# Performance work log

Measured on AMD Instinct MI355X. Metric: run time of the kernel, lower is better.

The kernel has to match this reference:

```python
import jax, jax.numpy as jnp
import numpy as np

B, S, D = 1, 2048, 1024
HK, DK = 8, 64
HV, DV = 16, 64
KEY_DIM = HK * DK          # 512
VAL_DIM = HV * DV          # 1024
CONV_DIM = 2 * KEY_DIM + VAL_DIM  # 2048
KW = 4                     # conv kernel width
E, TOPK, I_MOE = 8, 2, 512
EPS = 1e-6


def rms_norm(x, w, eps=EPS):
    xf = x.astype(jnp.float32)
    y = xf * jax.lax.rsqrt(jnp.mean(xf * xf, axis=-1, keepdims=True) + eps)
    return (y * (1.0 + w.astype(jnp.float32))).astype(x.dtype)


def l2norm(x, eps=1e-6):
    return x * jax.lax.rsqrt(jnp.sum(x * x, axis=-1, keepdims=True) + eps)


def setup_inputs() -> dict:
    key = jax.random.key(0)
    ks = jax.random.split(key, 16)
    n = lambda k, shp, s=0.02: (jax.random.normal(k, shp, dtype=jnp.float32) * s)
    return {
        'x': jax.random.normal(ks[0], (B, S, D), dtype=jnp.float32),
        'state': jnp.zeros((B, HV, DK, DV), dtype=jnp.float32),
        'conv_state': jnp.zeros((B, KW - 1, CONV_DIM), dtype=jnp.float32),
        'in_proj_qkv': n(ks[1], (D, CONV_DIM)),
        'in_proj_z': n(ks[2], (D, VAL_DIM)),
        'in_proj_a': n(ks[3], (D, HV)),
        'in_proj_b': n(ks[4], (D, HV)),
        'conv1d_weight': n(ks[5], (CONV_DIM, KW)),
        'dt_bias': jnp.ones((HV,), dtype=jnp.float32),
        'A_log': jnp.zeros((HV,), dtype=jnp.float32),
        'norm_weight': jnp.zeros((VAL_DIM,), dtype=jnp.float32),
        'out_proj': n(ks[6], (VAL_DIM, D)),
        'router_weight': n(ks[7], (E, D)),
        'expert_gate_up': n(ks[8], (E, 2 * I_MOE, D)),
        'expert_down': n(ks[9], (E, D, I_MOE)),
        'shared_gate': n(ks[10], (D, VAL_DIM)),
        'shared_up': n(ks[11], (D, VAL_DIM)),
        'shared_down': n(ks[12], (VAL_DIM, D)),
        'shared_expert_gate': n(ks[13], (D, 1)),
        'attention_norm_weight': jnp.zeros((D,), dtype=jnp.float32),
        'ffn_norm_weight': jnp.zeros((D,), dtype=jnp.float32),
        'linear_layer_idx': 0,
    }


def reference(x, state, conv_state, in_proj_qkv, in_proj_z, in_proj_a, in_proj_b,
              conv1d_weight, dt_bias, A_log, norm_weight, out_proj,
              router_weight, expert_gate_up, expert_down, shared_gate, shared_up,
              shared_down, shared_expert_gate, attention_norm_weight,
              ffn_norm_weight, linear_layer_idx):
    bsz, seqlen, dim = x.shape
    h = rms_norm(x, attention_norm_weight)

    # ---- Gated DeltaNet linear attention (prefill) ----
    qkv = h @ in_proj_qkv                    # [B,S,CONV_DIM]
    z = h @ in_proj_z                        # [B,S,VAL_DIM]
    a = h @ in_proj_a                        # [B,S,HV]
    b = h @ in_proj_b                        # [B,S,HV]

    # causal depthwise conv1d with rolling cache, then SiLU
    seq = jnp.concatenate([conv_state, qkv], axis=1)     # [B,S+KW-1,C]
    new_conv_state = seq[:, -(KW - 1):, :]
    xc = jnp.swapaxes(seq, 1, 2)                         # [B,C,S+KW-1]
    wk = conv1d_weight[:, None, :]                       # [C,1,KW]
    conv = jax.lax.conv_general_dilated(
        xc, wk, window_strides=(1,), padding='VALID',
        dimension_numbers=('NCH', 'OIH', 'NCH'), feature_group_count=CONV_DIM)
    qkv = jax.nn.silu(jnp.swapaxes(conv, 1, 2))          # [B,S,C]

    q, k, v = jnp.split(qkv, [KEY_DIM, 2 * KEY_DIM], axis=-1)
    q = l2norm(q.reshape(bsz, seqlen, HK, DK))
    k = l2norm(k.reshape(bsz, seqlen, HK, DK))
    rep = HV // HK
    q = jnp.repeat(q, rep, axis=2) * (DK ** -0.5)        # [B,S,HV,DK]
    k = jnp.repeat(k, rep, axis=2)
    v = v.reshape(bsz, seqlen, HV, DV)

    beta = jax.nn.sigmoid(b)                             # [B,S,HV]
    g = -jnp.exp(A_log) * jax.nn.softplus(a + dt_bias)   # log decay
    decay = jnp.exp(g)                                   # [B,S,HV]

    def step(St, inp):
        qt, kt, vt, dt_, bt = inp                        # per-token slices
        St = St * dt_[..., None, None]                   # gated decay
        mem = jnp.einsum('bhk,bhkv->bhv', kt, St)        # retrieve
        delta = (vt - mem) * bt[..., None]               # delta rule
        St = St + jnp.einsum('bhk,bhv->bhkv', kt, delta)
        ot = jnp.einsum('bhk,bhkv->bhv', qt, St)
        return St, ot

    xs = (jnp.moveaxis(q, 1, 0), jnp.moveaxis(k, 1, 0), jnp.moveaxis(v, 1, 0),
          jnp.moveaxis(decay, 1, 0), jnp.moveaxis(beta, 1, 0))
    new_state, o = jax.lax.scan(step, state, xs)
    o = jnp.moveaxis(o, 0, 1)                            # [B,S,HV,DV]

    # gated RMSNorm per value head, gate = silu(z)
    nw = (1.0 + norm_weight.astype(jnp.float32)).reshape(HV, DV)
    of = o.astype(jnp.float32)
    of = of * jax.lax.rsqrt(jnp.mean(of * of, axis=-1, keepdims=True) + EPS) * nw
    o = (of * jax.nn.silu(z.reshape(bsz, seqlen, HV, DV).astype(jnp.float32))).astype(x.dtype)
    attn_out = o.reshape(bsz, seqlen, VAL_DIM) @ out_proj
    x = x + attn_out

    # ---- MoE FFN with shared expert ----
    hf = rms_norm(x, ffn_norm_weight)
    t = hf.reshape(-1, dim)                              # [T,D]
    T = t.shape[0]
    logits = t @ router_weight.T                         # [T,E]
    probs = jax.nn.softmax(logits.astype(jnp.float32), axis=-1)
    vals, idx = jax.lax.top_k(probs, TOPK)
    vals = vals / jnp.sum(vals, axis=-1, keepdims=True)  # renormalized top-k
    wdense = jnp.zeros((T, E), jnp.float32).at[jnp.arange(T)[:, None], idx].set(vals)

    gu = jnp.einsum('td,eid->tei', t, expert_gate_up)    # [T,E,2I]
    gate, up = jnp.split(gu, 2, axis=-1)
    act = jax.nn.silu(gate) * up                         # [T,E,I]
    eo = jnp.einsum('tei,edi->ted', act, expert_down)    # [T,E,D]
    routed = jnp.einsum('ted,te->td', eo, wdense.astype(eo.dtype))

    sh = (jax.nn.silu(t @ shared_gate) * (t @ shared_up)) @ shared_down
    sh = sh * jax.nn.sigmoid(t @ shared_expert_gate)

    moe_out = (routed + sh).reshape(bsz, seqlen, dim)
    x = x + moe_out
    return x, new_state, new_conv_state
```

## Files before the change

### kernel.cpp

```cpp
#include <hip/hip_runtime.h>
#include <stdint.h>

typedef _Float16 f16;
typedef __attribute__((ext_vector_type(8))) _Float16 f16x8;
typedef __attribute__((ext_vector_type(4))) float f32x4;

#define DEV static __device__ __forceinline__

DEV float siluf(float x){ return x/(1.f+expf(-x)); }

__global__ __launch_bounds__(256)
void prep_kernel(const float* __restrict__ qkvw, const float* __restrict__ zw,
                 const float* __restrict__ opw, const float* __restrict__ sgw,
                 const float* __restrict__ suw, const float* __restrict__ sdw,
                 const float* __restrict__ guw, const float* __restrict__ dww,
                 f16* __restrict__ wqkvz, f16* __restrict__ wop, f16* __restrict__ wsgu,
                 f16* __restrict__ wsd, f16* __restrict__ wgu, f16* __restrict__ wdn)
{
  int b = blockIdx.x, tid = threadIdx.x;
  if (b >= 7168){
    if (b < 9216){
      size_t base = ((size_t)(b-7168))*4096 + (size_t)tid*16;
      long e = base>>20; long i = (base>>10)&1023; long d = base&1023;
      long ri = (i<512) ? ((i>>6)*128 + (i&63)) : (((i&511)>>6)*128 + 64 + (i&63));
      size_t dbase = ((size_t)e<<20) + ((size_t)ri<<10) + d;
      #pragma unroll
      for (int u=0;u<16;u++) wgu[dbase+u] = (f16)guw[base+u];
    } else {
      size_t base = ((size_t)(b-9216))*4096 + (size_t)tid*16;
      #pragma unroll
      for (int u=0;u<16;u++) wdn[base+u] = (f16)dww[base+u];
    }
    return;
  }
  const float* src; f16* dst; int N; int rowOff; int tile; int mode=0;
  if (b < 2048){ src=qkvw; dst=wqkvz; N=2048; rowOff=0;    tile=b; }
  else if (b < 3072){ src=zw;  dst=wqkvz; N=1024; rowOff=2048; tile=b-2048; }
  else if (b < 4096){ src=opw; dst=wop;  N=1024; rowOff=0;    tile=b-3072; }
  else if (b < 5120){ src=sgw; dst=wsgu; N=1024; rowOff=0;    tile=b-4096; mode=1; }
  else if (b < 6144){ src=suw; dst=wsgu; N=1024; rowOff=0;    tile=b-5120; mode=2; }
  else              { src=sdw; dst=wsd;  N=1024; rowOff=0;    tile=b-6144; }
  __shared__ float t32[32][33];
  int ntiles = N/32;
  int k0 = (tile/ntiles)*32, n0 = (tile%ntiles)*32;
  int rr = tid>>5, cc = tid&31;
  #pragma unroll
  for (int u=0;u<4;u++) t32[rr+u*8][cc] = src[(size_t)(k0+rr+u*8)*N + n0+cc];
  __syncthreads();
  #pragma unroll
  for (int u=0;u<4;u++){
    int vr = n0 + rr + u*8;
    int drow = rowOff + vr;
    if (mode==1) drow = (vr>>6)*128 + (vr&63);
    else if (mode==2) drow = (vr>>6)*128 + 64 + (vr&63);
    dst[(size_t)drow*1024 + k0+cc] = (f16)t32[cc][rr+u*8];
  }
}

__global__ __launch_bounds__(256)
void rms1(const float* __restrict__ xin, const float* __restrict__ w, f16* __restrict__ hb)
{
  __shared__ float red[4];
  int t = blockIdx.x, tid = threadIdx.x;
  const float* row = xin + (long)t*1024;
  float vals[4]; float ss=0.f;
  #pragma unroll
  for (int u=0;u<4;u++){ vals[u]=row[tid+256*u]; ss += vals[u]*vals[u]; }
  #pragma unroll
  for (int m=1;m<64;m<<=1) ss += __shfl_xor(ss,m);
  if ((tid&63)==0) red[tid>>6]=ss;
  __syncthreads();
  float sc = rsqrtf((red[0]+red[1]+red[2]+red[3])*(1.f/1024.f) + 1e-6f);
  #pragma unroll
  for (int u=0;u<4;u++){
    int d = tid+256*u;
    hb[(long)t*1024+d] = (f16)(vals[u]*sc*(1.f+w[d]));
  }
}

__global__ __launch_bounds__(256)
void rms2(const float* __restrict__ xin, const float* __restrict__ w,
          f16* __restrict__ hb, float* __restrict__ hf, int* __restrict__ cnt)
{
  __shared__ float red[4];
  int t = blockIdx.x, tid = threadIdx.x;
  if (blockIdx.x==0 && tid<8) cnt[tid]=0;
  const float* row = xin + (long)t*1024;
  float vals[4]; float ss=0.f;
  #pragma unroll
  for (int u=0;u<4;u++){ vals[u]=row[tid+256*u]; ss += vals[u]*vals[u]; }
  #pragma unroll
  for (int m=1;m<64;m<<=1) ss += __shfl_xor(ss,m);
  if ((tid&63)==0) red[tid>>6]=ss;
  __syncthreads();
  float sc = rsqrtf((red[0]+red[1]+red[2]+red[3])*(1.f/1024.f) + 1e-6f);
  #pragma unroll
  for (int u=0;u<4;u++){
    int d = tid+256*u;
    float v = vals[u]*sc*(1.f+w[d]);
    hb[(long)t*1024+d] = (f16)v;
    hf[(long)t*1024+d] = v;
  }
}

constexpr int GM_PLAIN=0, GM_ADDX=1, GM_GUF=2, GM_DOWN=3, GM_SHD=4, GM_SGUF=5;

template<int MODE>
__global__ __launch_bounds__(256)
void gemm_k(const f16* __restrict__ A, long strideA,
            const f16* __restrict__ B, long strideB,
            int K, int lda, int ldb,
            float* __restrict__ Cf, f16* __restrict__ Cb, int ldc, long strideCb,
            const float* __restrict__ xadd,
            const int* __restrict__ tok, const int* __restrict__ cntp,
            const int* __restrict__ slot, const float* __restrict__ wgt,
            const float* __restrict__ sig)
{
  constexpr bool FUSED = (MODE==GM_GUF || MODE==GM_SGUF);
  __shared__ f16 As[128*64];
  __shared__ f16 Bs[128*64];
  __shared__ int ltok[128];
  const int e = blockIdx.z;
  const int m0 = blockIdx.y*128, n0 = blockIdx.x*128;
  int cnt = 0x7fffffff;
  if (MODE==GM_GUF || MODE==GM_DOWN){
    cnt = cntp[e];
    if (m0 >= cnt) return;
  }
  const f16* Ap = A + (long)e*strideA;
  const f16* Bp = B + (long)e*strideB;
  const int tid = threadIdx.x, lane = tid&63, wv = tid>>6;
  if (MODE==GM_GUF){
    if (tid < 128){
      int p = m0 + tid;
      ltok[tid] = (p < cnt) ? tok[e*2048 + p] : 0;
    }
  }
  __syncthreads();
  const int srow = wv*8 + (lane>>3);
  const int scol = (lane&7)*8;
  long arow[4];
  #pragma unroll
  for (int i=0;i<4;i++){
    int r = srow + i*32;
    arow[i] = (MODE==GM_GUF) ? (long)ltok[r] : (long)(m0 + r);
  }
  f32x4 acc[4][4];
  #pragma unroll
  for (int mi=0;mi<4;mi++)
    #pragma unroll
    for (int ni=0;ni<4;ni++)
      acc[mi][ni] = (f32x4){0.f,0.f,0.f,0.f};

  for (int k0=0;k0<K;k0+=64){
    f16x8 av[4], bv[4];
    #pragma unroll
    for (int i=0;i<4;i++){
      int r = srow + i*32;
      av[i] = *(const f16x8*)(Ap + arow[i]*lda + k0 + scol);
      bv[i] = *(const f16x8*)(Bp + (long)(n0 + r)*ldb + k0 + scol);
    }
    __syncthreads();
    #pragma unroll
    for (int i=0;i<4;i++){
      int r = srow + i*32;
      *(f16x8*)&As[r*64 + scol] = av[i];
      *(f16x8*)&Bs[r*64 + scol] = bv[i];
    }
    __syncthreads();
    #pragma unroll
    for (int kk=0;kk<64;kk+=32){
      f16x8 af[4], bf[4];
      #pragma unroll
      for (int mi=0;mi<4;mi++){
        int row = (wv&1)*64 + mi*16 + (lane&15);
        af[mi] = *(const f16x8*)&As[row*64 + kk + (lane>>4)*8];
      }
      #pragma unroll
      for (int ni=0;ni<4;ni++){
        int row = FUSED ? (ni*32 + (wv>>1)*16 + (lane&15))
                        : ((wv>>1)*64 + ni*16 + (lane&15));
        bf[ni] = *(const f16x8*)&Bs[row*64 + kk + (lane>>4)*8];
      }
      #pragma unroll
      for (int mi=0;mi<4;mi++)
        #pragma unroll
        for (int ni=0;ni<4;ni++)
          acc[mi][ni] = __builtin_amdgcn_mfma_f32_16x16x32_f16(af[mi], bf[ni], acc[mi][ni], 0,0,0);
    }
  }
  if (FUSED){
    #pragma unroll
    for (int mi=0;mi<4;mi++){
      #pragma unroll
      for (int r=0;r<4;r++){
        int rowl = (wv&1)*64 + mi*16 + (lane>>4)*4 + r;
        int pos = m0 + rowl;
        #pragma unroll
        for (int pi=0;pi<2;pi++){
          int v = (n0>>1) + pi*32 + (wv>>1)*16 + (lane&15);
          float g = acc[mi][pi][r], u = acc[mi][pi+2][r];
          f16 a = (f16)(siluf(g)*u);
          if (MODE==GM_GUF) Cb[(long)e*strideCb + (long)pos*ldc + v] = a;
          else              Cb[(long)pos*ldc + v] = a;
        }
      }
    }
  } else {
    #pragma unroll
    for (int mi=0;mi<4;mi++){
      #pragma unroll
      for (int r=0;r<4;r++){
        int rowl = (wv&1)*64 + mi*16 + (lane>>4)*4 + r;
        int pos = m0 + rowl;
        int tk=0, sl=0; float wrow=0.f;
        if (MODE==GM_DOWN){
          if (pos < cnt){ tk = tok[e*2048+pos]; sl = slot[e*2048+pos]; wrow = wgt[e*2048+pos]; }
        }
        #pragma unroll
        for (int ni=0;ni<4;ni++){
          int col = n0 + (wv>>1)*64 + ni*16 + (lane&15);
          float v = acc[mi][ni][r];
          if (MODE==GM_PLAIN){
            Cf[(long)pos*ldc + col] = v;
          } else if (MODE==GM_ADDX){
            long idx = (long)pos*ldc + col;
            Cf[idx] = v + xadd[idx];
          } else if (MODE==GM_DOWN){
            if (pos < cnt) Cf[(long)sl*2097152 + (long)tk*1024 + col] = v*wrow;
          } else {
            Cf[(long)pos*ldc + col] = v*sig[pos];
          }
        }
      }
    }
  }
}

__global__ __launch_bounds__(256)
void ab_kernel(const f16* __restrict__ hb, const float* __restrict__ Wa,
               const float* __restrict__ Wbp, const float* __restrict__ dtb,
               const float* __restrict__ alog,
               float* __restrict__ gg, float* __restrict__ bbet)
{
  __shared__ float hrow[1024];
  __shared__ float part[256];
  int t = blockIdx.x, tid = threadIdx.x;
  #pragma unroll
  for (int u=0;u<4;u++){ int d = tid+256*u; hrow[d] = (float)hb[(long)t*1024+d]; }
  __syncthreads();
  int o = tid & 31;
  int r = tid >> 5;
  const float* W = (o<16) ? Wa : Wbp;
  int col = o & 15;
  float s = 0.f;
  for (int d=r; d<1024; d+=8) s += hrow[d]*W[d*16+col];
  part[tid] = s;
  __syncthreads();
  if (tid < 32){
    float tot=0.f;
    #pragma unroll
    for (int q=0;q<8;q++) tot += part[q*32 + tid];
    if (tid<16){
      float a = tot + dtb[tid];
      float sp = (a>20.f)? a : log1pf(expf(a));
      gg[t*16+tid] = -expf(alog[tid])*sp;
    } else {
      bbet[t*16+(tid-16)] = 1.f/(1.f+expf(-tot));
    }
  }
}

__global__ __launch_bounds__(256)
void conv_kernel(const float* __restrict__ qkvz, const float* __restrict__ cs,
                 const float* __restrict__ cw,
                 float* __restrict__ qn, float* __restrict__ kn,
                 float* __restrict__ vb, float* __restrict__ conv_out)
{
  int t = blockIdx.y;
  int c = blockIdx.x*256 + threadIdx.x;
  f32x4 w4 = *(const f32x4*)&cw[c*4];
  float acc = 0.f;
  #pragma unroll
  for (int j=0;j<4;j++){
    int s = t + j;
    float xv = (s<3) ? cs[s*2048 + c] : qkvz[(long)(s-3)*3072 + c];
    acc += w4[j]*xv;
  }
  float sv = siluf(acc);
  if (c < 1024){
    float ssq = sv*sv;
    #pragma unroll
    for (int m=1;m<64;m<<=1) ssq += __shfl_xor(ssq, m);
    float y = sv*rsqrtf(ssq + 1e-6f);
    if (c < 512) qn[(long)t*512 + c] = y*0.125f;
    else         kn[(long)t*512 + (c-512)] = y;
  } else {
    vb[(long)t*1024 + (c-1024)] = sv;
  }
  if (t >= 2045) conv_out[(t-2045)*2048 + c] = qkvz[(long)t*3072 + c];
}

__global__ __launch_bounds__(256)
void scan_pre(const float* __restrict__ kn, const float* __restrict__ vg,
              const float* __restrict__ gg, const float* __restrict__ bb,
              float* __restrict__ U0, f16* __restrict__ WbB,
              float* __restrict__ MT, float* __restrict__ NT)
{
  __shared__ f16 Kh[64][72];
  __shared__ f16 KrT[64][72];
  __shared__ f16 Amh[64][72];
  __shared__ float XT[64][68];
  __shared__ f16 Xh[64][72];
  __shared__ float cexp[64], gam[64], rlast[64], betl[64];
  const int task = blockIdx.x;
  const int h = task>>5, c = task&31, hk = h>>1;
  const int tid = threadIdx.x, lane = tid&63, wv = tid>>6;
  const long tb = (long)task*4096;

  if (wv==0){
    float g = gg[(c*64+lane)*16 + h];
    #pragma unroll
    for (int off=1; off<64; off<<=1){
      float tpp = __shfl_up(g, off);
      if (lane >= off) g += tpp;
    }
    cexp[lane] = g;
    betl[lane] = bb[(c*64+lane)*16 + h];
  }
  __syncthreads();
  if (tid<64){ gam[tid]=expf(cexp[tid]); rlast[tid]=expf(cexp[63]-cexp[tid]); }
  __syncthreads();
  for (int u=0;u<16;u++){
    int e2=u*256+tid; int t=e2>>6, x=e2&63;
    float kx = kn[(long)(c*64+t)*512 + hk*64 + x];
    Kh[t][x] = (f16)kx;
    KrT[x][t] = (f16)(rlast[t]*kx);
  }
  __syncthreads();
  {
    int mt = wv;
    for (int nt=0;nt<4;nt++){
      f32x4 acc = {0.f,0.f,0.f,0.f};
      #pragma unroll
      for (int kk=0;kk<64;kk+=32){
        f16x8 a = *(const f16x8*)&Kh[mt*16 + (lane&15)][kk + (lane>>4)*8];
        f16x8 bB = *(const f16x8*)&Kh[nt*16 + (lane&15)][kk + (lane>>4)*8];
        acc = __builtin_amdgcn_mfma_f32_16x16x32_f16(a, bB, acc, 0,0,0);
      }
      #pragma unroll
      for (int r=0;r<4;r++){
        int t = mt*16 + (lane>>4)*4 + r;
        int i = nt*16 + (lane&15);
        float v = (i<t) ? betl[t]*expf(cexp[t]-cexp[i])*acc[r] : 0.f;
        Amh[t][i] = (f16)v;
      }
    }
  }

  for (int pass=0; pass<2; pass++){
    for (int u=0;u<18;u++) ((f16*)Xh)[u*256+tid] = (f16)0.f;
    for (int u=0;u<16;u++){
      int e2=u*256+tid; int t=e2>>6, col=e2&63;
      float v = (pass==0) ? betl[t]*vg[(long)(c*64+t)*1024 + h*64 + col]
                          : betl[t]*gam[t]*kn[(long)(c*64+t)*512 + hk*64 + col];
      XT[col][t] = v;
    }
    __syncthreads();

    for (int b4=0;b4<4;b4++){
      if (tid<64){
        int col = tid;
        float xr[16];
        #pragma unroll
        for (int j=0;j<16;j+=4){
          f32x4 v = *(const f32x4*)&XT[col][b4*16+j];
          xr[j]=v.x; xr[j+1]=v.y; xr[j+2]=v.z; xr[j+3]=v.w;
        }
        #pragma unroll
        for (int t=1;t<16;t++){
          float a = xr[t];
          #pragma unroll
          for (int i=0;i<t;i++) a -= (float)Amh[b4*16+t][b4*16+i]*xr[i];
          xr[t] = a;
        }
        #pragma unroll
        for (int j=0;j<16;j+=4)
          *(f32x4*)&XT[col][b4*16+j] = (f32x4){xr[j],xr[j+1],xr[j+2],xr[j+3]};
        f16x8 h0, h1;
        #pragma unroll
        for (int j=0;j<8;j++){ h0[j]=(f16)xr[j]; h1[j]=(f16)xr[8+j]; }
        *(f16x8*)&Xh[col][b4*16]   = h0;
        *(f16x8*)&Xh[col][b4*16+8] = h1;
        if (pass==0){
          #pragma unroll
          for (int j=0;j<16;j++) U0[tb + (b4*16+j)*64 + col] = xr[j];
        } else {
          #pragma unroll
          for (int j=0;j<16;j++) WbB[tb + (b4*16+j)*64 + col] = (f16)xr[j];
        }
      }
      __syncthreads();
      if (b4<3){
        int ntiles = 4*(3-b4);
        for (int idx=wv; idx<ntiles; idx+=4){
          int mtile = idx & 3;
          int ntile = idx >> 2;
          int tp0 = 16*(b4+1) + ntile*16;
          f16x8 a  = *(const f16x8*)&Xh[mtile*16 + (lane&15)][b4*16 + (lane>>4)*8];
          f16x8 bB = *(const f16x8*)&Amh[tp0 + (lane&15)][b4*16 + (lane>>4)*8];
          f32x4 acc = {0.f,0.f,0.f,0.f};
          acc = __builtin_amdgcn_mfma_f32_16x16x32_f16(a, bB, acc, 0,0,0);
          #pragma unroll
          for (int r=0;r<4;r++){
            int colr = mtile*16 + (lane>>4)*4 + r;
            int tp = tp0 + (lane&15);
            XT[colr][tp] -= acc[r];
          }
        }
      }
      __syncthreads();
    }
    for (int idx=wv; idx<16; idx+=4){
      int mtile = idx & 3, ntile = idx >> 2;
      f32x4 acc = {0.f,0.f,0.f,0.f};
      #pragma unroll
      for (int kk=0;kk<64;kk+=32){
        f16x8 a  = *(const f16x8*)&Xh[mtile*16 + (lane&15)][kk + (lane>>4)*8];
        f16x8 bB = *(const f16x8*)&KrT[ntile*16 + (lane&15)][kk + (lane>>4)*8];
        acc = __builtin_amdgcn_mfma_f32_16x16x32_f16(a, bB, acc, 0,0,0);
      }
      #pragma unroll
      for (int r=0;r<4;r++){
        int m = mtile*16 + (lane>>4)*4 + r;
        int n = ntile*16 + (lane&15);
        if (pass==0) NT[tb + m*64 + n] = acc[r];
        else         MT[tb + m*64 + n] = ((n==m)?gam[63]:0.f) - acc[r];
      }
    }
    __syncthreads();
  }
}

__global__ __launch_bounds__(256)
void scan_seq(const float* __restrict__ st_in, const float* __restrict__ MT,
              const float* __restrict__ NT, float* __restrict__ SS,
              float* __restrict__ st_out)
{
  __shared__ float Mb[2][64*64];
  __shared__ float Nb[2][16*64];
  __shared__ float Sl[64][16];
  const int h = blockIdx.x>>2, vgq = blockIdx.x&3;
  const int tid = threadIdx.x, lane = tid&63, wv = tid>>6;
  const long hb0 = (long)h*32*4096;
  {
    int kx = tid>>2, j0 = (tid&3)*4;
    f32x4 s = *(const f32x4*)&st_in[h*4096 + kx*64 + vgq*16 + j0];
    *(f32x4*)&Sl[kx][j0] = s;
  }
  f32x4 mreg[4]; f32x4 nreg;
  #pragma unroll
  for (int u=0;u<4;u++) mreg[u] = *(const f32x4*)&MT[hb0 + (u*256+tid)*4];
  nreg = *(const f32x4*)&NT[hb0 + vgq*1024 + tid*4];
  #pragma unroll
  for (int u=0;u<4;u++) *(f32x4*)&Mb[0][(u*256+tid)*4] = mreg[u];
  *(f32x4*)&Nb[0][tid*4] = nreg;
  __syncthreads();

  const int kx = tid>>2, j0 = (tid&3)*4;
  for (int c=0;c<32;c++){
    const int buf = c&1;
    const long tb = hb0 + (long)c*4096;
    *(f32x4*)&SS[tb + kx*64 + vgq*16 + j0] = *(const f32x4*)&Sl[kx][j0];
    if (c<31){
      const long tb1 = tb + 4096;
      #pragma unroll
      for (int u=0;u<4;u++) mreg[u] = *(const f32x4*)&MT[tb1 + (u*256+tid)*4];
      nreg = *(const f32x4*)&NT[tb1 + vgq*1024 + tid*4];
    }
    f32x4 acc = {0.f,0.f,0.f,0.f};
    #pragma unroll 16
    for (int b=0;b<64;b++){
      float m = Mb[buf][b*64 + lane];
      f32x4 s4 = *(const f32x4*)&Sl[b][wv*4];
      acc.x += m*s4.x; acc.y += m*s4.y; acc.z += m*s4.z; acc.w += m*s4.w;
    }
    __syncthreads();
    Sl[lane][wv*4+0] = acc.x + Nb[buf][(wv*4+0)*64 + lane];
    Sl[lane][wv*4+1] = acc.y + Nb[buf][(wv*4+1)*64 + lane];
    Sl[lane][wv*4+2] = acc.z + Nb[buf][(wv*4+2)*64 + lane];
    Sl[lane][wv*4+3] = acc.w + Nb[buf][(wv*4+3)*64 + lane];
    if (c<31){
      #pragma unroll
      for (int u=0;u<4;u++) *(f32x4*)&Mb[buf^1][(u*256+tid)*4] = mreg[u];
      *(f32x4*)&Nb[buf^1][tid*4] = nreg;
    }
    __syncthreads();
  }
  *(f32x4*)&st_out[h*4096 + kx*64 + vgq*16 + j0] = *(const f32x4*)&Sl[kx][j0];
}

__global__ __launch_bounds__(256)
void scan_out(const float* __restrict__ qn, const float* __restrict__ kn,
              const float* __restrict__ gg, const float* __restrict__ U0,
              const f16* __restrict__ WbB, const float* __restrict__ SS,
              const float* __restrict__ qkvz, const float* __restrict__ nw,
              f16* __restrict__ obuf)
{
  __shared__ f16 Kh[64][72];
  __shared__ f16 Qh[64][72];
  __shared__ f16 Wbh[64][72];
  __shared__ f16 Bmh[64][72];
  __shared__ f16 STh[64][72];
  __shared__ f16 UTh[64][72];
  __shared__ float cexp[64], gam[64];
  const int task = blockIdx.x;
  const int h = task>>5, c = task&31, hk = h>>1;
  const int tid = threadIdx.x, lane = tid&63, wv = tid>>6;
  const long tb = (long)task*4096;

  if (wv==0){
    float g = gg[(c*64+lane)*16 + h];
    #pragma unroll
    for (int off=1; off<64; off<<=1){
      float tpp = __shfl_up(g, off);
      if (lane >= off) g += tpp;
    }
    cexp[lane]=g; gam[lane]=expf(g);
  }
  __syncthreads();
  for (int u=0;u<16;u++){
    int e2=u*256+tid; int t=e2>>6, x=e2&63;
    float kx = kn[(long)(c*64+t)*512 + hk*64 + x];
    float qx = qn[(long)(c*64+t)*512 + hk*64 + x];
    Kh[t][x]=(f16)kx;
    Qh[t][x]=(f16)qx;
    Wbh[t][x] = WbB[tb + t*64 + x];
    STh[x][t] = (f16)SS[tb + t*64 + x];
  }
  __syncthreads();
  {
    int mt = wv;
    for (int nt=0;nt<4;nt++){
      f32x4 acc={0.f,0.f,0.f,0.f};
      #pragma unroll
      for (int kk=0;kk<64;kk+=32){
        f16x8 a  = *(const f16x8*)&Qh[mt*16+(lane&15)][kk+(lane>>4)*8];
        f16x8 bB = *(const f16x8*)&Kh[nt*16+(lane&15)][kk+(lane>>4)*8];
        acc = __builtin_amdgcn_mfma_f32_16x16x32_f16(a,bB,acc,0,0,0);
      }
      #pragma unroll
      for (int r=0;r<4;r++){
        int t = mt*16+(lane>>4)*4+r;
        int i = nt*16+(lane&15);
        float v = (i<=t)? expf(cexp[t]-cexp[i])*acc[r] : 0.f;
        Bmh[t][i] = (f16)v;
      }
    }
  }
  __syncthreads();
  {
    int mt = wv;
    for (int nt=0;nt<4;nt++){
      f32x4 acc={0.f,0.f,0.f,0.f};
      #pragma unroll
      for (int kk=0;kk<64;kk+=32){
        f16x8 a  = *(const f16x8*)&Wbh[mt*16+(lane&15)][kk+(lane>>4)*8];
        f16x8 bB = *(const f16x8*)&STh[nt*16+(lane&15)][kk+(lane>>4)*8];
        acc = __builtin_amdgcn_mfma_f32_16x16x32_f16(a,bB,acc,0,0,0);
      }
      #pragma unroll
      for (int r=0;r<4;r++){
        int t = mt*16+(lane>>4)*4+r;
        int v = nt*16+(lane&15);
        float uv = U0[tb + t*64 + v] - acc[r];
        UTh[v][t] = (f16)uv;
      }
    }
    for (int u=0;u<16;u++){
      int e2=u*256+tid; int t=e2>>6, x=e2&63;
      Qh[t][x] = (f16)(gam[t]*(float)Qh[t][x]);
    }
  }
  __syncthreads();
  {
    int mt = wv;
    f32x4 acc[4];
    for (int nt=0;nt<4;nt++){
      acc[nt]=(f32x4){0.f,0.f,0.f,0.f};
      #pragma unroll
      for (int kk=0;kk<64;kk+=32){
        f16x8 a  = *(const f16x8*)&Qh[mt*16+(lane&15)][kk+(lane>>4)*8];
        f16x8 bB = *(const f16x8*)&STh[nt*16+(lane&15)][kk+(lane>>4)*8];
        acc[nt] = __builtin_amdgcn_mfma_f32_16x16x32_f16(a,bB,acc[nt],0,0,0);
      }
      #pragma unroll
      for (int kk=0;kk<64;kk+=32){
        f16x8 a  = *(const f16x8*)&Bmh[mt*16+(lane&15)][kk+(lane>>4)*8];
        f16x8 bB = *(const f16x8*)&UTh[nt*16+(lane&15)][kk+(lane>>4)*8];
        acc[nt] = __builtin_amdgcn_mfma_f32_16x16x32_f16(a,bB,acc[nt],0,0,0);
      }
    }
    #pragma unroll
    for (int r=0;r<4;r++){
      float ss = acc[0][r]*acc[0][r] + acc[1][r]*acc[1][r]
               + acc[2][r]*acc[2][r] + acc[3][r]*acc[3][r];
      ss += __shfl_xor(ss,1); ss += __shfl_xor(ss,2);
      ss += __shfl_xor(ss,4); ss += __shfl_xor(ss,8);
      float scale = rsqrtf(ss*(1.f/64.f) + 1e-6f);
      int t = mt*16 + (lane>>4)*4 + r;
      int tg = c*64 + t;
      #pragma unroll
      for (int nt=0;nt<4;nt++){
        int v = nt*16 + (lane&15);
        float z = qkvz[(long)tg*3072 + 2048 + h*64 + v];
        float val = acc[nt][r]*scale*(1.f+nw[h*64+v])*siluf(z);
        obuf[(long)tg*1024 + h*64 + v] = (f16)val;
      }
    }
  }
}

__global__ __launch_bounds__(64)
void router_k(const float* __restrict__ hff, const float* __restrict__ rw,
              const float* __restrict__ seg,
              int* __restrict__ cnt, int* __restrict__ etok, int* __restrict__ eslot,
              float* __restrict__ ew, float* __restrict__ sig)
{
  int t = blockIdx.x; int lane = threadIdx.x;
  const float* row = hff + (long)t*1024;
  float p[9];
  #pragma unroll
  for (int e=0;e<9;e++) p[e]=0.f;
  for (int rdx=0; rdx<16; rdx++){
    int d = lane + 64*rdx;
    float xv = row[d];
    #pragma unroll
    for (int e=0;e<8;e++) p[e] += xv*rw[e*1024+d];
    p[8] += xv*seg[d];
  }
  #pragma unroll
  for (int e=0;e<9;e++)
    #pragma unroll
    for (int m=1;m<64;m<<=1) p[e] += __shfl_xor(p[e], m);
  if (lane==0){
    float mx = p[0];
    for (int e=1;e<8;e++) mx = fmaxf(mx,p[e]);
    float pe[8];
    for (int e=0;e<8;e++) pe[e]=expf(p[e]-mx);
    int i0=0; for (int e=1;e<8;e++) if (pe[e]>pe[i0]) i0=e;
    int i1 = (i0==0)?1:0;
    for (int e=0;e<8;e++) if (e!=i0 && pe[e]>pe[i1]) i1=e;
    float denom = pe[i0]+pe[i1];
    float w0 = pe[i0]/denom, w1 = pe[i1]/denom;
    int p0 = atomicAdd(&cnt[i0],1);
    etok[i0*2048+p0]=t; eslot[i0*2048+p0]=0; ew[i0*2048+p0]=w0;
    int p1 = atomicAdd(&cnt[i1],1);
    etok[i1*2048+p1]=t; eslot[i1*2048+p1]=1; ew[i1*2048+p1]=w1;
    sig[t] = 1.f/(1.f+expf(-p[8]));
  }
}

__global__ __launch_bounds__(256)
void fin_kernel(const float* __restrict__ x2, const float* __restrict__ eo2,
                const float* __restrict__ sh, float* __restrict__ outx)
{
  long idx = (long)blockIdx.x*256 + threadIdx.x;
  outx[idx] = x2[idx] + eo2[idx] + eo2[idx + 2097152] + sh[idx];
}

extern "C" void kernel_launch(void* const* d_in, const int* in_sizes, int n_in,
                              void* d_out, int out_size, void* d_ws, size_t ws_size,
                              hipStream_t stream)
{
  (void)in_sizes; (void)n_in; (void)out_size; (void)ws_size;
  const float* x      = (const float*)d_in[0];
  const float* state  = (const float*)d_in[1];
  const float* cstate = (const float*)d_in[2];
  const float* w_qkv  = (const float*)d_in[3];
  const float* w_z    = (const float*)d_in[4];
  const float* w_a    = (const float*)d_in[5];
  const float* w_b    = (const float*)d_in[6];
  const float* convw  = (const float*)d_in[7];
  const float* dtb    = (const float*)d_in[8];
  const float* alog   = (const float*)d_in[9];
  const float* normw  = (const float*)d_in[10];
  const float* w_op   = (const float*)d_in[11];
  const float* rw     = (const float*)d_in[12];
  const float* w_gu   = (const float*)d_in[13];
  const float* w_dn   = (const float*)d_in[14];
  const float* w_sg   = (const float*)d_in[15];
  const float* w_su   = (const float*)d_in[16];
  const float* w_sd   = (const float*)d_in[17];
  const float* w_seg  = (const float*)d_in[18];
  const float* anw    = (const float*)d_in[19];
  const float* fnw    = (const float*)d_in[20];

  char* ws = (char*)d_ws;
  size_t off = 0;
  auto alloc = [&](size_t bytes)->char*{
    char* p = ws + off; off += (bytes + 255) & ~(size_t)255; return p;
  };
  f16*  wTqkvz = (f16*)alloc((size_t)3072*1024*2);
  f16*  wTop   = (f16*)alloc((size_t)1024*1024*2);
  f16*  wTsgu  = (f16*)alloc((size_t)2048*1024*2);
  f16*  wTsd   = (f16*)alloc((size_t)1024*1024*2);
  f16*  wGUc   = (f16*)alloc((size_t)8*1024*1024*2);
  f16*  wDNc   = (f16*)alloc((size_t)8*1024*512*2);
  f16*  hbuf   = (f16*)alloc((size_t)2048*1024*2);
  float* qkvz  = (float*)alloc((size_t)2048*3072*4);
  float* qn    = (float*)alloc((size_t)2048*512*4);
  float* kn    = (float*)alloc((size_t)2048*512*4);
  float* vb    = (float*)alloc((size_t)2048*1024*4);
  float* gg    = (float*)alloc((size_t)2048*16*4);
  float* bbuf  = (float*)alloc((size_t)2048*16*4);
  float* U0    = (float*)alloc((size_t)512*4096*4);
  f16*  WbB    = (f16*)alloc((size_t)512*4096*2);
  float* MT    = (float*)alloc((size_t)512*4096*4);
  float* NT    = (float*)alloc((size_t)512*4096*4);
  float* SS    = (float*)alloc((size_t)512*4096*4);
  float* x2    = (float*)alloc((size_t)2048*1024*4);
  f16*  hfb    = (f16*)alloc((size_t)2048*1024*2);
  float* hff   = (float*)alloc((size_t)2048*1024*4);
  int*  cnt    = (int*)alloc(256);
  int*  etok   = (int*)alloc((size_t)8*2048*4);
  int*  eslot  = (int*)alloc((size_t)8*2048*4);
  float* ew    = (float*)alloc((size_t)8*2048*4);
  float* sigb  = (float*)alloc((size_t)2048*4);
  f16*  obuf  = hbuf;
  f16*  sactb = (f16*)qn;
  float* shb  = vb;
  f16*  actb  = (f16*)U0;
  float* eo2  = (float*)((char*)U0 + (size_t)16777216);

  float* out_x = (float*)d_out;
  float* out_state = out_x + 2097152;
  float* out_conv = out_state + 65536;

  prep_kernel<<<10240, 256, 0, stream>>>(w_qkv, w_z, w_op, w_sg, w_su, w_sd, w_gu, w_dn,
                                         wTqkvz, wTop, wTsgu, wTsd, wGUc, wDNc);
  rms1<<<2048, 256, 0, stream>>>(x, anw, hbuf);
  gemm_k<GM_PLAIN><<<dim3(24,16,1), 256, 0, stream>>>(hbuf, 0, wTqkvz, 0, 1024, 1024, 1024,
        qkvz, nullptr, 3072, 0, nullptr, nullptr, nullptr, nullptr, nullptr, nullptr);
  ab_kernel<<<2048, 256, 0, stream>>>(hbuf, w_a, w_b, dtb, alog, gg, bbuf);
  conv_kernel<<<dim3(8,2048), 256, 0, stream>>>(qkvz, cstate, convw, qn, kn, vb, out_conv);
  scan_pre<<<512, 256, 0, stream>>>(kn, vb, gg, bbuf, U0, WbB, MT, NT);
  scan_seq<<<64, 256, 0, stream>>>(state, MT, NT, SS, out_state);
  scan_out<<<512, 256, 0, stream>>>(qn, kn, gg, U0, WbB, SS, qkvz, normw, obuf);
  gemm_k<GM_ADDX><<<dim3(8,16,1), 256, 0, stream>>>(obuf, 0, wTop, 0, 1024, 1024, 1024,
        x2, nullptr, 1024, 0, x, nullptr, nullptr, nullptr, nullptr, nullptr);
  rms2<<<2048, 256, 0, stream>>>(x2, fnw, hfb, hff, cnt);
  router_k<<<2048, 64, 0, stream>>>(hff, rw, w_seg, cnt, etok, eslot, ew, sigb);
  gemm_k<GM_GUF><<<dim3(8,16,8), 256, 0, stream>>>(hfb, 0, wGUc, (long)1024*1024, 1024, 1024, 1024,
        nullptr, actb, 512, (long)2048*512, nullptr, etok, cnt, nullptr, nullptr, nullptr);
  gemm_k<GM_DOWN><<<dim3(8,16,8), 256, 0, stream>>>(actb, (long)2048*512, wDNc, (long)1024*512,
        512, 512, 512,
        eo2, nullptr, 1024, 0, nullptr, etok, cnt, eslot, ew, nullptr);
  gemm_k<GM_SGUF><<<dim3(16,16,1), 256, 0, stream>>>(hfb, 0, wTsgu, 0, 1024, 1024, 1024,
        nullptr, sactb, 1024, 0, nullptr, nullptr, nullptr, nullptr, nullptr, nullptr);
  gemm_k<GM_SHD><<<dim3(8,16,1), 256, 0, stream>>>(sactb, 0, wTsd, 0, 1024, 1024, 1024,
        shb, nullptr, 1024, 0, nullptr, nullptr, nullptr, nullptr, nullptr, sigb);
  fin_kernel<<<8192, 256, 0, stream>>>(x2, eo2, shb, out_x);
}
```

Baseline: 540.5 us.

## Fuse router into second RMSNorm and stage GEMM tiles via direct global-to-LDS loads

Merges the MoE router (logits, softmax, top-2, token bucketing, shared-expert sigmoid) into the rms2 kernel. This removes one launch and the fp32 normalized-activation round trip through global memory, and the counter reset moves to a memset. The GEMM kernel now uses global_load_lds to copy A/B tiles straight into LDS instead of going through registers, which cuts register pressure and VGPR traffic. Each k-step still has two barriers and there is no double buffering, so load latency is still not overlapped.

```diff
diff --git a/kernel.cpp b/kernel.cpp
--- a/kernel.cpp
+++ b/kernel.cpp
@@ -8,6 +8,12 @@
 #define DEV static __device__ __forceinline__
 
 DEV float siluf(float x){ return x/(1.f+expf(-x)); }
+
+DEV void load_lds16(const f16* g, f16* l){
+  __builtin_amdgcn_global_load_lds(
+      (const __attribute__((address_space(1))) void*)g,
+      (__attribute__((address_space(3))) void*)l, 16, 0, 0);
+}
 
 __global__ __launch_bounds__(256)
 void prep_kernel(const float* __restrict__ qkvw, const float* __restrict__ zw,
@@ -80,26 +86,62 @@
 
 __global__ __launch_bounds__(256)
 void rms2(const float* __restrict__ xin, const float* __restrict__ w,
-          f16* __restrict__ hb, float* __restrict__ hf, int* __restrict__ cnt)
+          const float* __restrict__ rw, const float* __restrict__ seg,
+          f16* __restrict__ hb,
+          int* __restrict__ cnt, int* __restrict__ etok, int* __restrict__ eslot,
+          float* __restrict__ ew, float* __restrict__ sig)
 {
   __shared__ float red[4];
-  int t = blockIdx.x, tid = threadIdx.x;
-  if (blockIdx.x==0 && tid<8) cnt[tid]=0;
+  __shared__ float rbuf[9][4];
+  int t = blockIdx.x, tid = threadIdx.x, lane = tid&63, wv = tid>>6;
   const float* row = xin + (long)t*1024;
   float vals[4]; float ss=0.f;
   #pragma unroll
   for (int u=0;u<4;u++){ vals[u]=row[tid+256*u]; ss += vals[u]*vals[u]; }
   #pragma unroll
   for (int m=1;m<64;m<<=1) ss += __shfl_xor(ss,m);
-  if ((tid&63)==0) red[tid>>6]=ss;
+  if (lane==0) red[wv]=ss;
   __syncthreads();
   float sc = rsqrtf((red[0]+red[1]+red[2]+red[3])*(1.f/1024.f) + 1e-6f);
+  float p[9];
+  #pragma unroll
+  for (int e=0;e<9;e++) p[e]=0.f;
   #pragma unroll
   for (int u=0;u<4;u++){
     int d = tid+256*u;
     float v = vals[u]*sc*(1.f+w[d]);
     hb[(long)t*1024+d] = (f16)v;
-    hf[(long)t*1024+d] = v;
+    #pragma unroll
+    for (int e=0;e<8;e++) p[e] += v*rw[e*1024+d];
+    p[8] += v*seg[d];
+  }
+  #pragma unroll
+  for (int e=0;e<9;e++)
+    #pragma unroll
+    for (int m=1;m<64;m<<=1) p[e] += __shfl_xor(p[e], m);
+  if (lane==0){
+    #pragma unroll
+    for (int e=0;e<9;e++) rbuf[e][wv]=p[e];
+  }
+  __syncthreads();
+  if (tid==0){
+    float pl[9];
+    #pragma unroll
+    for (int e=0;e<9;e++) pl[e]=rbuf[e][0]+rbuf[e][1]+rbuf[e][2]+rbuf[e][3];
+    float mx = pl[0];
+    for (int e=1;e<8;e++) mx = fmaxf(mx,pl[e]);
+    float pe[8];
+    for (int e=0;e<8;e++) pe[e]=expf(pl[e]-mx);
+    int i0=0; for (int e=1;e<8;e++) if (pe[e]>pe[i0]) i0=e;
+    int i1 = (i0==0)?1:0;
+    for (int e=0;e<8;e++) if (e!=i0 && pe[e]>pe[i1]) i1=e;
+    float denom = pe[i0]+pe[i1];
+    float w0 = pe[i0]/denom, w1 = pe[i1]/denom;
+    int p0 = atomicAdd(&cnt[i0],1);
+    etok[i0*2048+p0]=t; eslot[i0*2048+p0]=0; ew[i0*2048+p0]=w0;
+    int p1 = atomicAdd(&cnt[i1],1);
+    etok[i1*2048+p1]=t; eslot[i1*2048+p1]=1; ew[i1*2048+p1]=w1;
+    sig[t] = 1.f/(1.f+expf(-pl[8]));
   }
 }
 
@@ -135,8 +177,8 @@
       int p = m0 + tid;
       ltok[tid] = (p < cnt) ? tok[e*2048 + p] : 0;
     }
-  }
-  __syncthreads();
+    __syncthreads();
+  }
   const int srow = wv*8 + (lane>>3);
   const int scol = (lane&7)*8;
   long arow[4];
@@ -153,19 +195,12 @@
       acc[mi][ni] = (f32x4){0.f,0.f,0.f,0.f};
 
   for (int k0=0;k0<K;k0+=64){
-    f16x8 av[4], bv[4];
+    __syncthreads();
     #pragma unroll
     for (int i=0;i<4;i++){
       int r = srow + i*32;
-      av[i] = *(const f16x8*)(Ap + arow[i]*lda + k0 + scol);
-      bv[i] = *(const f16x8*)(Bp + (long)(n0 + r)*ldb + k0 + scol);
-    }
-    __syncthreads();
-    #pragma unroll
-    for (int i=0;i<4;i++){
-      int r = srow + i*32;
-      *(f16x8*)&As[r*64 + scol] = av[i];
-      *(f16x8*)&Bs[r*64 + scol] = bv[i];
+      load_lds16(Ap + arow[i]*lda + k0 + scol, &As[r*64 + scol]);
+      load_lds16(Bp + (long)(n0 + r)*ldb + k0 + scol, &Bs[r*64 + scol]);
     }
     __syncthreads();
     #pragma unroll
@@ -621,46 +656,6 @@
   }
 }
 
-__global__ __launch_bounds__(64)
-void router_k(const float* __restrict__ hff, const float* __restrict__ rw,
-              const float* __restrict__ seg,
-              int* __restrict__ cnt, int* __restrict__ etok, int* __restrict__ eslot,
-              float* __restrict__ ew, float* __restrict__ sig)
-{
-  int t = blockIdx.x; int lane = threadIdx.x;
-  const float* row = hff + (long)t*1024;
-  float p[9];
-  #pragma unroll
-  for (int e=0;e<9;e++) p[e]=0.f;
-  for (int rdx=0; rdx<16; rdx++){
-    int d = lane + 64*rdx;
-    float xv = row[d];
-    #pragma unroll
-    for (int e=0;e<8;e++) p[e] += xv*rw[e*1024+d];
-    p[8] += xv*seg[d];
-  }
-  #pragma unroll
-  for (int e=0;e<9;e++)
-    #pragma unroll
-    for (int m=1;m<64;m<<=1) p[e] += __shfl_xor(p[e], m);
-  if (lane==0){
-    float mx = p[0];
-    for (int e=1;e<8;e++) mx = fmaxf(mx,p[e]);
-    float pe[8];
-    for (int e=0;e<8;e++) pe[e]=expf(p[e]-mx);
-    int i0=0; for (int e=1;e<8;e++) if (pe[e]>pe[i0]) i0=e;
-    int i1 = (i0==0)?1:0;
-    for (int e=0;e<8;e++) if (e!=i0 && pe[e]>pe[i1]) i1=e;
-    float denom = pe[i0]+pe[i1];
-    float w0 = pe[i0]/denom, w1 = pe[i1]/denom;
-    int p0 = atomicAdd(&cnt[i0],1);
-    etok[i0*2048+p0]=t; eslot[i0*2048+p0]=0; ew[i0*2048+p0]=w0;
-    int p1 = atomicAdd(&cnt[i1],1);
-    etok[i1*2048+p1]=t; eslot[i1*2048+p1]=1; ew[i1*2048+p1]=w1;
-    sig[t] = 1.f/(1.f+expf(-p[8]));
-  }
-}
-
 __global__ __launch_bounds__(256)
 void fin_kernel(const float* __restrict__ x2, const float* __restrict__ eo2,
                 const float* __restrict__ sh, float* __restrict__ outx)
@@ -721,7 +716,6 @@
   float* SS    = (float*)alloc((size_t)512*4096*4);
   float* x2    = (float*)alloc((size_t)2048*1024*4);
   f16*  hfb    = (f16*)alloc((size_t)2048*1024*2);
-  float* hff   = (float*)alloc((size_t)2048*1024*4);
   int*  cnt    = (int*)alloc(256);
   int*  etok   = (int*)alloc((size_t)8*2048*4);
   int*  eslot  = (int*)alloc((size_t)8*2048*4);
@@ -737,6 +731,7 @@
   float* out_state = out_x + 2097152;
   float* out_conv = out_state + 65536;
 
+  hipMemsetAsync((void*)cnt, 0, 64, stream);
   prep_kernel<<<10240, 256, 0, stream>>>(w_qkv, w_z, w_op, w_sg, w_su, w_sd, w_gu, w_dn,
                                          wTqkvz, wTop, wTsgu, wTsd, wGUc, wDNc);
   rms1<<<2048, 256, 0, stream>>>(x, anw, hbuf);
@@ -749,8 +744,7 @@
   scan_out<<<512, 256, 0, stream>>>(qn, kn, gg, U0, WbB, SS, qkvz, normw, obuf);
   gemm_k<GM_ADDX><<<dim3(8,16,1), 256, 0, stream>>>(obuf, 0, wTop, 0, 1024, 1024, 1024,
         x2, nullptr, 1024, 0, x, nullptr, nullptr, nullptr, nullptr, nullptr);
-  rms2<<<2048, 256, 0, stream>>>(x2, fnw, hfb, hff, cnt);
-  router_k<<<2048, 64, 0, stream>>>(hff, rw, w_seg, cnt, etok, eslot, ew, sigb);
+  rms2<<<2048, 256, 0, stream>>>(x2, fnw, rw, w_seg, hfb, cnt, etok, eslot, ew, sigb);
   gemm_k<GM_GUF><<<dim3(8,16,8), 256, 0, stream>>>(hfb, 0, wGUc, (long)1024*1024, 1024, 1024, 1024,
         nullptr, actb, 512, (long)2048*512, nullptr, etok, cnt, nullptr, nullptr, nullptr);
   gemm_k<GM_DOWN><<<dim3(8,16,8), 256, 0, stream>>>(actb, (long)2048*512, wDNc, (long)1024*512,
```

After: 516.0 us. 4.5% less time.
